# Kernel tuning notes

Measured on AMD Instinct MI355X. Metric: run time of the kernel, lower is better.

## Reference

```python
import jax, jax.numpy as jnp
import numpy as np

N = 50000   # nodes
E = 500000  # edges
F = 256     # node feature dim
ED = 64     # edge feature dim
H = 128     # hidden channels
O = 32      # out channels
NEG_SLOPE = 0.2
EPS = 1e-16


def setup_inputs() -> dict:
    key = jax.random.key(0)
    ks = jax.random.split(key, 16)
    s = 0.05
    return {
        "x": jax.random.normal(ks[0], (N, F), jnp.float32),
        "edge_index": jax.random.randint(ks[1], (2, E), 0, N, dtype=jnp.int32),
        "edge_attr": jax.random.normal(ks[2], (E, ED), jnp.float32),
        # layer 1 (embed): F -> H
        "W1": jax.random.normal(ks[3], (F, H), jnp.float32) * s,
        "att_src1": jax.random.normal(ks[4], (H,), jnp.float32) * s,
        "att_dst1": jax.random.normal(ks[5], (H,), jnp.float32) * s,
        "We1": jax.random.normal(ks[6], (ED, H), jnp.float32) * s,
        "att_edge1": jax.random.normal(ks[7], (H,), jnp.float32) * s,
        "b1": jnp.zeros((H,), jnp.float32),
        # layer 2 (classifier): H -> O
        "W2": jax.random.normal(ks[8], (H, O), jnp.float32) * s,
        "att_src2": jax.random.normal(ks[9], (O,), jnp.float32) * s,
        "att_dst2": jax.random.normal(ks[10], (O,), jnp.float32) * s,
        "We2": jax.random.normal(ks[11], (ED, O), jnp.float32) * s,
        "att_edge2": jax.random.normal(ks[12], (O,), jnp.float32) * s,
        "b2": jnp.zeros((O,), jnp.float32),
    }


def _add_self_loops_mean(src, dst, ea, n):
    # PyG add_self_loops(fill_value='mean'): self-loop edge_attr = mean of
    # incoming edge_attr per target node (0 for isolated nodes).
    ones = jnp.ones((ea.shape[0],), ea.dtype)
    cnt = jax.ops.segment_sum(ones, dst, num_segments=n)
    summ = jax.ops.segment_sum(ea, dst, num_segments=n)  # [n, ED]
    mean = summ / jnp.maximum(cnt, 1.0)[:, None]
    loop = jnp.arange(n, dtype=src.dtype)
    return (jnp.concatenate([src, loop]),
            jnp.concatenate([dst, loop]),
            jnp.concatenate([ea, mean], axis=0))


def _gat_conv(x, src, dst, ea, W, a_src, a_dst, We, a_edge, b):
    n = x.shape[0]
    src, dst, ea = _add_self_loops_mean(src, dst, ea, n)
    h = x @ W                       # [n, C]
    he = ea @ We                    # [E', C]
    a_s = h @ a_src                 # [n]
    a_d = h @ a_dst                 # [n]
    a_e = he @ a_edge               # [E']
    alpha = a_s[src] + a_d[dst] + a_e
    alpha = jax.nn.leaky_relu(alpha, NEG_SLOPE)
    # segment softmax over incoming edges of each target node
    m = jax.ops.segment_max(alpha, dst, num_segments=n)
    ex = jnp.exp(alpha - m[dst])
    denom = jax.ops.segment_sum(ex, dst, num_segments=n)
    coef = ex / (denom[dst] + EPS)
    out = jax.ops.segment_sum(coef[:, None] * h[src], dst, num_segments=n)
    return out + b


def reference(x, edge_index, edge_attr,
              W1, att_src1, att_dst1, We1, att_edge1, b1,
              W2, att_src2, att_dst2, We2, att_edge2, b2):
    src, dst = edge_index[0], edge_index[1]
    x1 = _gat_conv(x, src, dst, edge_attr, W1, att_src1, att_dst1, We1, att_edge1, b1)
    h = jax.nn.relu(x1)  # Dropout(0.5) is identity in eval mode
    out = _gat_conv(h, src, dst, edge_attr, W2, att_src2, att_dst2, We2, att_edge2, b2)
    return (out, h)
```

## Files before the change

### kernel.cpp

```cpp
#include <hip/hip_runtime.h>

#define N_NODES 50000
#define N_EDGES 500000
#define F_DIM 256
#define ED_DIM 64
#define H_DIM 128
#define O_DIM 32
#define NEG_SLOPE 0.2f
#define EPS_F 1e-16f

#define EB 2048

typedef __attribute__((ext_vector_type(8))) short short8;
typedef __attribute__((ext_vector_type(4))) float floatx4;

__device__ __forceinline__ unsigned short f2bf(float f) {
    union { float f; unsigned u; } c; c.f = f;
    unsigned u = c.u;
    return (unsigned short)((u + 0x7fffu + ((u >> 16) & 1u)) >> 16);
}
__device__ __forceinline__ float bf2f_lo(unsigned u) { return __uint_as_float(u << 16); }
__device__ __forceinline__ float bf2f_hi(unsigned u) { return __uint_as_float(u & 0xffff0000u); }
__device__ __forceinline__ float leaky(float a) { return a > 0.f ? a : a * NEG_SLOPE; }
__device__ __forceinline__ float dot4(float4 a, float4 b) {
    return a.x * b.x + a.y * b.y + a.z * b.z + a.w * b.w;
}

__global__ void k_prep(const float* __restrict__ We1, const float* __restrict__ aev1,
                       const float* __restrict__ We2, const float* __restrict__ aev2,
                       float* __restrict__ wv1, float* __restrict__ wv2,
                       const float* __restrict__ W1, const float* __restrict__ W2,
                       const float* __restrict__ as2v, const float* __restrict__ ad2v,
                       float* __restrict__ was2, float* __restrict__ wad2,
                       unsigned short* __restrict__ W1T, unsigned short* __restrict__ W2T,
                       int* __restrict__ cnt) {
    if (blockIdx.x == 32) {
        int t = threadIdx.x;
        if (t < 64) {
            float s = 0.f;
            for (int c = 0; c < H_DIM; c++) s += We1[t * H_DIM + c] * aev1[c];
            wv1[t] = s;
        } else if (t < 128) {
            int k = t - 64;
            float s = 0.f;
            for (int c = 0; c < O_DIM; c++) s += We2[k * O_DIM + c] * aev2[c];
            wv2[k] = s;
        } else {
            int c = t - 128;
            float s = 0.f, d = 0.f;
            for (int o = 0; o < O_DIM; o++) {
                float w = W2[c * O_DIM + o];
                s += w * as2v[o];
                d += w * ad2v[o];
            }
            was2[c] = s; wad2[c] = d;
        }
        return;
    }
    int gid = blockIdx.x * 256 + threadIdx.x;
    const int stride = 32 * 256;
    for (int i = gid; i < N_NODES; i += stride) cnt[i] = 0;
    for (int i = gid; i < H_DIM * F_DIM; i += stride) {
        int n = i >> 8, k = i & 255;
        W1T[i] = f2bf(W1[k * H_DIM + n]);
    }
    for (int i = gid; i < O_DIM * H_DIM; i += stride) {
        int n = i >> 7, k = i & 127;
        W2T[i] = f2bf(W2[k * O_DIM + n]);
    }
}

__global__ __launch_bounds__(256) void k_edge_ae(
        const float* __restrict__ ea, const int* __restrict__ dst,
        const float* __restrict__ wv1, const float* __restrict__ wv2,
        float2* __restrict__ ae12, int* __restrict__ cnt) {
    int tid = threadIdx.x;
    int wave = tid >> 6, lane = tid & 63;
    int sub = lane & 3, eg = lane >> 2;
    float4 w1[4], w2[4];
#pragma unroll
    for (int j = 0; j < 4; j++) {
        w1[j] = ((const float4*)wv1)[sub * 4 + j];
        w2[j] = ((const float4*)wv2)[sub * 4 + j];
    }
    int g0 = (blockIdx.x * 4 + wave) * 16 + eg;
    const int stride = EB * 64;
    for (int e = g0; e < N_EDGES; e += stride) {
        const float4* row = (const float4*)(ea + (size_t)e * ED_DIM + sub * 16);
        float4 q0 = row[0], q1 = row[1], q2 = row[2], q3 = row[3];
        float s1 = dot4(q0, w1[0]) + dot4(q1, w1[1]) + dot4(q2, w1[2]) + dot4(q3, w1[3]);
        float s2 = dot4(q0, w2[0]) + dot4(q1, w2[1]) + dot4(q2, w2[2]) + dot4(q3, w2[3]);
        s1 += __shfl_xor(s1, 1); s2 += __shfl_xor(s2, 1);
        s1 += __shfl_xor(s1, 2); s2 += __shfl_xor(s2, 2);
        if (sub == 0) {
            ae12[e] = make_float2(s1, s2);
            atomicAdd(&cnt[dst[e]], 1);
        }
    }
}

__global__ __launch_bounds__(256) void k_gemm1(const float* __restrict__ A,
        const unsigned short* __restrict__ BT,
        const float* __restrict__ asv, const float* __restrict__ adv,
        unsigned short* __restrict__ Hb, float* __restrict__ a_s, float* __restrict__ a_d, int M) {
    __shared__ unsigned short As[128 * 40];
    __shared__ unsigned short Bs[128 * 40];
    int tid = threadIdx.x;
    int wave = tid >> 6, lane = tid & 63;
    int q = lane >> 4, r = lane & 15;
    int bm0 = blockIdx.x * 128;
    floatx4 acc[2][8];
#pragma unroll
    for (int a = 0; a < 2; a++)
#pragma unroll
        for (int b = 0; b < 8; b++) acc[a][b] = (floatx4){0.f, 0.f, 0.f, 0.f};

    int rr = tid >> 3;
    int kc = tid & 7;
    for (int k0 = 0; k0 < 256; k0 += 32) {
#pragma unroll
        for (int i = 0; i < 4; i++) {
            int row = rr + 32 * i;
            int gr = bm0 + row;
            float4 v = make_float4(0.f, 0.f, 0.f, 0.f);
            if (gr < M) v = *(const float4*)(A + (size_t)gr * 256 + k0 + kc * 4);
            unsigned lo = (unsigned)f2bf(v.x) | ((unsigned)f2bf(v.y) << 16);
            unsigned hi = (unsigned)f2bf(v.z) | ((unsigned)f2bf(v.w) << 16);
            *(uint2*)&As[row * 40 + kc * 4] = make_uint2(lo, hi);
        }
#pragma unroll
        for (int i = 0; i < 2; i++) {
            int idx = tid + 256 * i;
            int n = idx >> 2, ck = idx & 3;
            *(uint4*)&Bs[n * 40 + ck * 8] = *(const uint4*)(BT + n * 256 + k0 + ck * 8);
        }
        __syncthreads();
        short8 af[2], bf[8];
#pragma unroll
        for (int rt = 0; rt < 2; rt++)
            af[rt] = *(const short8*)&As[(wave * 32 + rt * 16 + r) * 40 + q * 8];
#pragma unroll
        for (int nt = 0; nt < 8; nt++)
            bf[nt] = *(const short8*)&Bs[(nt * 16 + r) * 40 + q * 8];
#pragma unroll
        for (int rt = 0; rt < 2; rt++)
#pragma unroll
            for (int nt = 0; nt < 8; nt++)
                acc[rt][nt] = __builtin_amdgcn_mfma_f32_16x16x32_bf16(af[rt], bf[nt], acc[rt][nt], 0, 0, 0);
        __syncthreads();
    }
#pragma unroll
    for (int rt = 0; rt < 2; rt++) {
        int rowb = bm0 + wave * 32 + rt * 16 + q * 4;
        float ps[4] = {0.f, 0.f, 0.f, 0.f}, pd[4] = {0.f, 0.f, 0.f, 0.f};
#pragma unroll
        for (int nt = 0; nt < 8; nt++) {
            int col = nt * 16 + r;
            float av = asv[col], dv = adv[col];
#pragma unroll
            for (int reg = 0; reg < 4; reg++) {
                float v = acc[rt][nt][reg];
                if (rowb + reg < M) Hb[(size_t)(rowb + reg) * 128 + col] = f2bf(v);
                ps[reg] += v * av;
                pd[reg] += v * dv;
            }
        }
#pragma unroll
        for (int reg = 0; reg < 4; reg++) {
#pragma unroll
            for (int off = 1; off < 16; off <<= 1) {
                ps[reg] += __shfl_xor(ps[reg], off);
                pd[reg] += __shfl_xor(pd[reg], off);
            }
        }
        if (r == 0) {
#pragma unroll
            for (int reg = 0; reg < 4; reg++) {
                if (rowb + reg < M) { a_s[rowb + reg] = ps[reg]; a_d[rowb + reg] = pd[reg]; }
            }
        }
    }
}

__global__ void k_scan1(const int* __restrict__ cnt, int* __restrict__ bsum, int n) {
    __shared__ int sh[256];
    int b = blockIdx.x, t = threadIdx.x;
    int base = b * 1024;
    int s = 0;
    for (int j = 0; j < 4; j++) {
        int idx = base + t * 4 + j;
        if (idx < n) s += cnt[idx];
    }
    sh[t] = s; __syncthreads();
    for (int o = 128; o > 0; o >>= 1) {
        if (t < o) sh[t] += sh[t + o];
        __syncthreads();
    }
    if (t == 0) bsum[b] = sh[0];
}

__global__ void k_scan2(const int* __restrict__ bsum, int* __restrict__ bpre,
                        int* __restrict__ offs, int nb, int n) {
    if (threadIdx.x == 0) {
        int run = 0;
        for (int b = 0; b < nb; b++) { bpre[b] = run; run += bsum[b]; }
        offs[n] = run;
    }
}

__global__ void k_scan3(const int* __restrict__ cnt, const int* __restrict__ bpre,
                        int* __restrict__ offs, int* __restrict__ cursor, int n) {
    __shared__ int sh[256];
    int b = blockIdx.x, t = threadIdx.x;
    int base = b * 1024;
    int v[4]; int s = 0;
    for (int j = 0; j < 4; j++) {
        int idx = base + t * 4 + j;
        v[j] = (idx < n) ? cnt[idx] : 0;
        s += v[j];
    }
    sh[t] = s; __syncthreads();
    for (int o = 1; o < 256; o <<= 1) {
        int x = (t >= o) ? sh[t - o] : 0;
        __syncthreads();
        sh[t] += x;
        __syncthreads();
    }
    int texcl = sh[t] - s + bpre[b];
    int run = 0;
    for (int j = 0; j < 4; j++) {
        int idx = base + t * 4 + j;
        if (idx < n) { offs[idx] = texcl + run; cursor[idx] = texcl + run; }
        run += v[j];
    }
}

__global__ __launch_bounds__(256) void k_scatter(const int* __restrict__ src, const int* __restrict__ dst,
                          const float2* __restrict__ ae12, const float* __restrict__ a_s1,
                          int* __restrict__ cursor, float4* __restrict__ csr) {
    int e = blockIdx.x * blockDim.x + threadIdx.x;
    if (e >= N_EDGES) return;
    int s = src[e];
    int d = dst[e];
    float2 a = ae12[e];
    float as = a_s1[s];
    int p = atomicAdd(&cursor[d], 1);
    csr[p] = make_float4(__int_as_float(s), a.x, a.y, as);
}

template <bool RELU>
__global__ __launch_bounds__(256) void k_agg128(const unsigned short* __restrict__ h,
                         const float* __restrict__ a_s, const float* __restrict__ a_d,
                         const int* __restrict__ offs, const float4* __restrict__ csr,
                         const float* __restrict__ bias,
                         const float* __restrict__ was2, const float* __restrict__ wad2,
                         float* __restrict__ a_s2, float* __restrict__ a_d2,
                         float* __restrict__ out) {
    int wave = threadIdx.x >> 6, lane = threadIdx.x & 63;
    int i = blockIdx.x * 4 + wave;
    int r = lane & 15;
    int g = lane >> 4;
    int rs = offs[i], re = offs[i + 1];
    int deg = re - rs;
    float adl = a_d[i];
    float4 acc0 = {0.f, 0.f, 0.f, 0.f}, acc1 = {0.f, 0.f, 0.f, 0.f};
    float dsum = 0.f, sum_ae = 0.f;

#define P128(EL)                                                              \
    {                                                                         \
        float4 c = csr[EL];            \
        int s = __float_as_int(c.x);                                          \
        float aev = c.y;                                                      \
        float ex = __expf(leaky(c.w + adl + aev));                            \
        if (r == 0) { dsum += ex; sum_ae += aev; }                            \
        uint4 hv = *(const uint4*)(h + (size_t)s * 128 + r * 8);              \
        acc0.x += ex * bf2f_lo(hv.x); acc0.y += ex * bf2f_hi(hv.x);           \
        acc0.z += ex * bf2f_lo(hv.y); acc0.w += ex * bf2f_hi(hv.y);           \
        acc1.x += ex * bf2f_lo(hv.z); acc1.y += ex * bf2f_hi(hv.z);           \
        acc1.z += ex * bf2f_lo(hv.w); acc1.w += ex * bf2f_hi(hv.w);           \
    }

    int el = rs + g;
    for (; el + 4 < re; el += 8) { P128(el); P128(el + 4); }
    if (el < re) P128(el);
#undef P128

#pragma unroll
    for (int o = 1; o < 64; o <<= 1) {
        dsum += __shfl_xor(dsum, o);
        sum_ae += __shfl_xor(sum_ae, o);
    }

    float loop_ae = sum_ae / (float)(deg > 1 ? deg : 1);
    float al = leaky(a_s[i] + adl + loop_ae);
    float exs = __expf(al);
    float* a0 = (float*)&acc0; float* a1 = (float*)&acc1;
#pragma unroll
    for (int c = 0; c < 4; c++) {
        a0[c] += __shfl_xor(a0[c], 16); a0[c] += __shfl_xor(a0[c], 32);
        a1[c] += __shfl_xor(a1[c], 16); a1[c] += __shfl_xor(a1[c], 32);
    }
    if (g == 0) {
        float inv = 1.0f / (dsum + exs + EPS_F);
        uint4 hv = *(const uint4*)(h + (size_t)i * 128 + r * 8);
        const float4* bp = (const float4*)bias;
        float4 b0 = bp[r * 2], b1 = bp[r * 2 + 1];
        float4 o0, o1;
        o0.x = (a0[0] + exs * bf2f_lo(hv.x)) * inv + b0.x;
        o0.y = (a0[1] + exs * bf2f_hi(hv.x)) * inv + b0.y;
        o0.z = (a0[2] + exs * bf2f_lo(hv.y)) * inv + b0.z;
        o0.w = (a0[3] + exs * bf2f_hi(hv.y)) * inv + b0.w;
        o1.x = (a1[0] + exs * bf2f_lo(hv.z)) * inv + b1.x;
        o1.y = (a1[1] + exs * bf2f_hi(hv.z)) * inv + b1.y;
        o1.z = (a1[2] + exs * bf2f_lo(hv.w)) * inv + b1.z;
        o1.w = (a1[3] + exs * bf2f_hi(hv.w)) * inv + b1.w;
        if (RELU) {
            o0.x = fmaxf(o0.x, 0.f); o0.y = fmaxf(o0.y, 0.f); o0.z = fmaxf(o0.z, 0.f); o0.w = fmaxf(o0.w, 0.f);
            o1.x = fmaxf(o1.x, 0.f); o1.y = fmaxf(o1.y, 0.f); o1.z = fmaxf(o1.z, 0.f); o1.w = fmaxf(o1.w, 0.f);
        }
        float4* op = (float4*)(out + (size_t)i * 128);
        op[r * 2] = o0;
        op[r * 2 + 1] = o1;
        float4 wsa = ((const float4*)was2)[r * 2], wsb = ((const float4*)was2)[r * 2 + 1];
        float4 wda = ((const float4*)wad2)[r * 2], wdb = ((const float4*)wad2)[r * 2 + 1];
        float ps = dot4(o0, wsa) + dot4(o1, wsb);
        float pd = dot4(o0, wda) + dot4(o1, wdb);
#pragma unroll
        for (int o = 1; o < 16; o <<= 1) {
            ps += __shfl_xor(ps, o);
            pd += __shfl_xor(pd, o);
        }
        if (r == 0) { a_s2[i] = ps; a_d2[i] = pd; }
    }
}

__global__ __launch_bounds__(256) void k_gemm2(const float* __restrict__ A,
        const unsigned short* __restrict__ BT,
        unsigned short* __restrict__ Hb, int M) {
    __shared__ unsigned short As[128 * 40];
    __shared__ unsigned short Bs[32 * 40];
    int tid = threadIdx.x;
    int wave = tid >> 6, lane = tid & 63;
    int q = lane >> 4, r = lane & 15;
    int bm0 = blockIdx.x * 128;
    floatx4 acc[2][2];
#pragma unroll
    for (int a = 0; a < 2; a++)
#pragma unroll
        for (int b = 0; b < 2; b++) acc[a][b] = (floatx4){0.f, 0.f, 0.f, 0.f};

    int rr = tid >> 3;
    int kc = tid & 7;
    for (int k0 = 0; k0 < 128; k0 += 32) {
#pragma unroll
        for (int i = 0; i < 4; i++) {
            int row = rr + 32 * i;
            int gr = bm0 + row;
            float4 v = make_float4(0.f, 0.f, 0.f, 0.f);
            if (gr < M) v = *(const float4*)(A + (size_t)gr * 128 + k0 + kc * 4);
            unsigned lo = (unsigned)f2bf(v.x) | ((unsigned)f2bf(v.y) << 16);
            unsigned hi = (unsigned)f2bf(v.z) | ((unsigned)f2bf(v.w) << 16);
            *(uint2*)&As[row * 40 + kc * 4] = make_uint2(lo, hi);
        }
        if (tid < 128) {
            int n = tid >> 2, ck = tid & 3;
            *(uint4*)&Bs[n * 40 + ck * 8] = *(const uint4*)(BT + n * 128 + k0 + ck * 8);
        }
        __syncthreads();
        short8 af[2], bf[2];
#pragma unroll
        for (int rt = 0; rt < 2; rt++)
            af[rt] = *(const short8*)&As[(wave * 32 + rt * 16 + r) * 40 + q * 8];
#pragma unroll
        for (int nt = 0; nt < 2; nt++)
            bf[nt] = *(const short8*)&Bs[(nt * 16 + r) * 40 + q * 8];
#pragma unroll
        for (int rt = 0; rt < 2; rt++)
#pragma unroll
            for (int nt = 0; nt < 2; nt++)
                acc[rt][nt] = __builtin_amdgcn_mfma_f32_16x16x32_bf16(af[rt], bf[nt], acc[rt][nt], 0, 0, 0);
        __syncthreads();
    }
#pragma unroll
    for (int rt = 0; rt < 2; rt++) {
        int rowb = bm0 + wave * 32 + rt * 16 + q * 4;
#pragma unroll
        for (int nt = 0; nt < 2; nt++) {
            int col = nt * 16 + r;
#pragma unroll
            for (int reg = 0; reg < 4; reg++) {
                if (rowb + reg < M) Hb[(size_t)(rowb + reg) * 32 + col] = f2bf(acc[rt][nt][reg]);
            }
        }
    }
}

__global__ __launch_bounds__(256) void k_agg32(const unsigned short* __restrict__ h,
                        const float* __restrict__ a_s, const float* __restrict__ a_d,
                        const int* __restrict__ offs, const float4* __restrict__ csr,
                        const float* __restrict__ bias,
                        float* __restrict__ out) {
    int wave = threadIdx.x >> 6, lane = threadIdx.x & 63;
    int i = blockIdx.x * 4 + wave;
    int r = lane & 7;
    int g = lane >> 3;
    int rs = offs[i], re = offs[i + 1];
    int deg = re - rs;
    float adl = a_d[i];
    float4 acc = {0.f, 0.f, 0.f, 0.f};
    float dsum = 0.f, sum_ae = 0.f;

#define P32(EL)                                                               \
    {                                                                         \
        float4 c = csr[EL];                                                   \
        int s = __float_as_int(c.x);                                          \
        float aev = c.z;                                                      \
        float ex = __expf(leaky(a_s[s] + adl + aev));                         \
        if (r == 0) { dsum += ex; sum_ae += aev; }                            \
        uint2 hv = *(const uint2*)(h + (size_t)s * 32 + r * 4);               \
        acc.x += ex * bf2f_lo(hv.x); acc.y += ex * bf2f_hi(hv.x);             \
        acc.z += ex * bf2f_lo(hv.y); acc.w += ex * bf2f_hi(hv.y);             \
    }

    int el = rs + g;
    for (; el + 8 < re; el += 16) { P32(el); P32(el + 8); }
    if (el < re) P32(el);
#undef P32

#pragma unroll
    for (int o = 1; o < 64; o <<= 1) {
        dsum += __shfl_xor(dsum, o);
        sum_ae += __shfl_xor(sum_ae, o);
    }

    float loop_ae = sum_ae / (float)(deg > 1 ? deg : 1);
    float al = leaky(a_s[i] + adl + loop_ae);
    float exs = __expf(al);
#pragma unroll
    for (int o = 8; o < 64; o <<= 1) {
        acc.x += __shfl_xor(acc.x, o); acc.y += __shfl_xor(acc.y, o);
        acc.z += __shfl_xor(acc.z, o); acc.w += __shfl_xor(acc.w, o);
    }
    if (g == 0) {
        float inv = 1.0f / (dsum + exs + EPS_F);
        uint2 hv = *(const uint2*)(h + (size_t)i * 32 + r * 4);
        float4 bv = ((const float4*)bias)[r];
        float4 ov;
        ov.x = (acc.x + exs * bf2f_lo(hv.x)) * inv + bv.x;
        ov.y = (acc.y + exs * bf2f_hi(hv.x)) * inv + bv.y;
        ov.z = (acc.z + exs * bf2f_lo(hv.y)) * inv + bv.z;
        ov.w = (acc.w + exs * bf2f_hi(hv.y)) * inv + bv.w;
        ((float4*)(out + (size_t)i * 32))[r] = ov;
    }
}

extern "C" void kernel_launch(void* const* d_in, const int* in_sizes, int n_in,
                              void* d_out, int out_size, void* d_ws, size_t ws_size,
                              hipStream_t stream) {
    const float* x    = (const float*)d_in[0];
    const int* ei     = (const int*)d_in[1];
    const float* ea   = (const float*)d_in[2];
    const float* W1   = (const float*)d_in[3];
    const float* as1v = (const float*)d_in[4];
    const float* ad1v = (const float*)d_in[5];
    const float* We1  = (const float*)d_in[6];
    const float* aev1 = (const float*)d_in[7];
    const float* b1   = (const float*)d_in[8];
    const float* W2   = (const float*)d_in[9];
    const float* as2v = (const float*)d_in[10];
    const float* ad2v = (const float*)d_in[11];
    const float* We2  = (const float*)d_in[12];
    const float* aev2 = (const float*)d_in[13];
    const float* b2   = (const float*)d_in[14];

    const int* src = ei;
    const int* dst = ei + N_EDGES;

    char* w = (char*)d_ws;
    size_t off = 0;
    auto alloc = [&](size_t bytes) -> void* {
        void* p = w + off;
        off += bytes;
        off = (off + 255) & ~(size_t)255;
        return p;
    };
    unsigned short* h1b = (unsigned short*)alloc((size_t)N_NODES * H_DIM * 2);
    unsigned short* h2b = (unsigned short*)alloc((size_t)N_NODES * O_DIM * 2);
    float2* ae12   = (float2*)alloc((size_t)N_EDGES * 8);
    int* cnt       = (int*)alloc((size_t)N_NODES * 4);
    int* offs      = (int*)alloc((size_t)(N_NODES + 1) * 4);
    int* cursor    = (int*)alloc((size_t)N_NODES * 4);
    float4* csr    = (float4*)alloc((size_t)N_EDGES * 16);
    int* bsum      = (int*)alloc(64 * 4);
    int* bpre      = (int*)alloc(64 * 4);
    float* wv1     = (float*)alloc(64 * 4);
    float* wv2     = (float*)alloc(64 * 4);
    float* was2    = (float*)alloc(128 * 4);
    float* wad2    = (float*)alloc(128 * 4);
    float* a_s1    = (float*)alloc((size_t)N_NODES * 4);
    float* a_d1    = (float*)alloc((size_t)N_NODES * 4);
    float* a_s2    = (float*)alloc((size_t)N_NODES * 4);
    float* a_d2    = (float*)alloc((size_t)N_NODES * 4);
    unsigned short* W1T = (unsigned short*)alloc((size_t)H_DIM * F_DIM * 2);
    unsigned short* W2T = (unsigned short*)alloc((size_t)O_DIM * H_DIM * 2);

    k_prep<<<33, 256, 0, stream>>>(We1, aev1, We2, aev2, wv1, wv2, W1, W2,
                                   as2v, ad2v, was2, wad2, W1T, W2T, cnt);

    k_edge_ae<<<EB, 256, 0, stream>>>(ea, dst, wv1, wv2, ae12, cnt);

    k_gemm1<<<(N_NODES + 127) / 128, 256, 0, stream>>>(x, W1T, as1v, ad1v,
                                                       h1b, a_s1, a_d1, N_NODES);

    int nb = (N_NODES + 1023) / 1024;
    k_scan1<<<nb, 256, 0, stream>>>(cnt, bsum, N_NODES);
    k_scan2<<<1, 64, 0, stream>>>(bsum, bpre, offs, nb, N_NODES);
    k_scan3<<<nb, 256, 0, stream>>>(cnt, bpre, offs, cursor, N_NODES);

    k_scatter<<<(N_EDGES + 255) / 256, 256, 0, stream>>>(src, dst, ae12, a_s1,
                                                         cursor, csr);

    float* out = (float*)d_out;
    float* h_out = out + (size_t)N_NODES * O_DIM;

    k_agg128<true><<<(N_NODES + 3) / 4, 256, 0, stream>>>(h1b, a_s1, a_d1, offs,
                                                          csr, b1, was2, wad2,
                                                          a_s2, a_d2, h_out);

    k_gemm2<<<(N_NODES + 127) / 128, 256, 0, stream>>>(h_out, W2T, h2b, N_NODES);

    k_agg32<<<(N_NODES + 3) / 4, 256, 0, stream>>>(h2b, a_s2, a_d2, offs,
                                                   csr, b2, out);
}
```

Measured before the change: 379.3 us.

## Fuse second-layer GEMM into aggregation kernel and merge scan passes

The layer-2 projection (h @ W2) now happens inside the first aggregation kernel. W2 is staged in shared memory, each node's ReLU output goes through a per-wave shared buffer, and a dot product produces the bf16 h2 row directly, so the separate MFMA GEMM kernel and its re-read of h_out are gone. The aggregation kernels become persistent grid-stride loops over a fixed grid of 2048 blocks. The single-thread scan2 kernel is folded into scan3, with each block summing the earlier block totals through a wave shuffle. The fused GEMM runs as scalar FP32 FMAs instead of matrix cores, and it adds a block-wide barrier per node iteration.

```diff
diff --git a/kernel.cpp b/kernel.cpp
--- a/kernel.cpp
+++ b/kernel.cpp
@@ -10,6 +10,7 @@
 #define EPS_F 1e-16f
 
 #define EB 2048
+#define AB 2048
 
 typedef __attribute__((ext_vector_type(8))) short short8;
 typedef __attribute__((ext_vector_type(4))) float floatx4;
@@ -32,7 +33,7 @@
                        const float* __restrict__ W1, const float* __restrict__ W2,
                        const float* __restrict__ as2v, const float* __restrict__ ad2v,
                        float* __restrict__ was2, float* __restrict__ wad2,
-                       unsigned short* __restrict__ W1T, unsigned short* __restrict__ W2T,
+                       unsigned short* __restrict__ W1T,
                        int* __restrict__ cnt) {
     if (blockIdx.x == 32) {
         int t = threadIdx.x;
@@ -64,10 +65,6 @@
         int n = i >> 8, k = i & 255;
         W1T[i] = f2bf(W1[k * H_DIM + n]);
     }
-    for (int i = gid; i < O_DIM * H_DIM; i += stride) {
-        int n = i >> 7, k = i & 127;
-        W2T[i] = f2bf(W2[k * O_DIM + n]);
-    }
 }
 
 __global__ __launch_bounds__(256) void k_edge_ae(
@@ -199,25 +196,23 @@
     if (t == 0) bsum[b] = sh[0];
 }
 
-__global__ void k_scan2(const int* __restrict__ bsum, int* __restrict__ bpre,
-                        int* __restrict__ offs, int nb, int n) {
-    if (threadIdx.x == 0) {
-        int run = 0;
-        for (int b = 0; b < nb; b++) { bpre[b] = run; run += bsum[b]; }
-        offs[n] = run;
-    }
-}
-
-__global__ void k_scan3(const int* __restrict__ cnt, const int* __restrict__ bpre,
-                        int* __restrict__ offs, int* __restrict__ cursor, int n) {
+__global__ void k_scan3(const int* __restrict__ cnt, const int* __restrict__ bsum,
+                        int* __restrict__ offs, int* __restrict__ cursor, int n, int nb) {
     __shared__ int sh[256];
+    __shared__ int bpre_sh;
     int b = blockIdx.x, t = threadIdx.x;
+    if (t < 64) {
+        int v = (t < b) ? bsum[t] : 0;
+#pragma unroll
+        for (int o = 1; o < 64; o <<= 1) v += __shfl_xor(v, o);
+        if (t == 0) bpre_sh = v;
+    }
     int base = b * 1024;
-    int v[4]; int s = 0;
+    int v4[4]; int s = 0;
     for (int j = 0; j < 4; j++) {
         int idx = base + t * 4 + j;
-        v[j] = (idx < n) ? cnt[idx] : 0;
-        s += v[j];
+        v4[j] = (idx < n) ? cnt[idx] : 0;
+        s += v4[j];
     }
     sh[t] = s; __syncthreads();
     for (int o = 1; o < 256; o <<= 1) {
@@ -226,13 +221,14 @@
         sh[t] += x;
         __syncthreads();
     }
-    int texcl = sh[t] - s + bpre[b];
+    int texcl = sh[t] - s + bpre_sh;
     int run = 0;
     for (int j = 0; j < 4; j++) {
         int idx = base + t * 4 + j;
         if (idx < n) { offs[idx] = texcl + run; cursor[idx] = texcl + run; }
-        run += v[j];
-    }
+        run += v4[j];
+    }
+    if (b == nb - 1 && t == 255) offs[n] = bpre_sh + sh[255];
 }
 
 __global__ __launch_bounds__(256) void k_scatter(const int* __restrict__ src, const int* __restrict__ dst,
@@ -248,23 +244,32 @@
     csr[p] = make_float4(__int_as_float(s), a.x, a.y, as);
 }
 
-template <bool RELU>
 __global__ __launch_bounds__(256) void k_agg128(const unsigned short* __restrict__ h,
                          const float* __restrict__ a_s, const float* __restrict__ a_d,
                          const int* __restrict__ offs, const float4* __restrict__ csr,
                          const float* __restrict__ bias,
                          const float* __restrict__ was2, const float* __restrict__ wad2,
+                         const float* __restrict__ W2,
                          float* __restrict__ a_s2, float* __restrict__ a_d2,
+                         unsigned short* __restrict__ h2b,
                          float* __restrict__ out) {
-    int wave = threadIdx.x >> 6, lane = threadIdx.x & 63;
-    int i = blockIdx.x * 4 + wave;
+    __shared__ float W2s[128 * 32];
+    __shared__ float xsh[4][128];
+    int tid = threadIdx.x;
+    for (int idx = tid; idx < 128 * 32; idx += 256) W2s[idx] = W2[idx];
+    __syncthreads();
+    int wave = tid >> 6, lane = tid & 63;
     int r = lane & 15;
     int g = lane >> 4;
-    int rs = offs[i], re = offs[i + 1];
-    int deg = re - rs;
-    float adl = a_d[i];
-    float4 acc0 = {0.f, 0.f, 0.f, 0.f}, acc1 = {0.f, 0.f, 0.f, 0.f};
-    float dsum = 0.f, sum_ae = 0.f;
+    int ch = lane & 31, half = lane >> 5;
+
+    for (int i0 = blockIdx.x * 4; i0 < N_NODES; i0 += gridDim.x * 4) {
+        int i = i0 + wave;
+        int rs = offs[i], re = offs[i + 1];
+        int deg = re - rs;
+        float adl = a_d[i];
+        float4 acc0 = {0.f, 0.f, 0.f, 0.f}, acc1 = {0.f, 0.f, 0.f, 0.f};
+        float dsum = 0.f, sum_ae = 0.f;
 
 #define P128(EL)                                                              \
     {                                                                         \
@@ -280,117 +285,68 @@
         acc1.z += ex * bf2f_lo(hv.w); acc1.w += ex * bf2f_hi(hv.w);           \
     }
 
-    int el = rs + g;
-    for (; el + 4 < re; el += 8) { P128(el); P128(el + 4); }
-    if (el < re) P128(el);
+        int el = rs + g;
+        for (; el + 4 < re; el += 8) { P128(el); P128(el + 4); }
+        if (el < re) P128(el);
 #undef P128
 
 #pragma unroll
-    for (int o = 1; o < 64; o <<= 1) {
-        dsum += __shfl_xor(dsum, o);
-        sum_ae += __shfl_xor(sum_ae, o);
-    }
-
-    float loop_ae = sum_ae / (float)(deg > 1 ? deg : 1);
-    float al = leaky(a_s[i] + adl + loop_ae);
-    float exs = __expf(al);
-    float* a0 = (float*)&acc0; float* a1 = (float*)&acc1;
-#pragma unroll
-    for (int c = 0; c < 4; c++) {
-        a0[c] += __shfl_xor(a0[c], 16); a0[c] += __shfl_xor(a0[c], 32);
-        a1[c] += __shfl_xor(a1[c], 16); a1[c] += __shfl_xor(a1[c], 32);
-    }
-    if (g == 0) {
-        float inv = 1.0f / (dsum + exs + EPS_F);
-        uint4 hv = *(const uint4*)(h + (size_t)i * 128 + r * 8);
-        const float4* bp = (const float4*)bias;
-        float4 b0 = bp[r * 2], b1 = bp[r * 2 + 1];
-        float4 o0, o1;
-        o0.x = (a0[0] + exs * bf2f_lo(hv.x)) * inv + b0.x;
-        o0.y = (a0[1] + exs * bf2f_hi(hv.x)) * inv + b0.y;
-        o0.z = (a0[2] + exs * bf2f_lo(hv.y)) * inv + b0.z;
-        o0.w = (a0[3] + exs * bf2f_hi(hv.y)) * inv + b0.w;
-        o1.x = (a1[0] + exs * bf2f_lo(hv.z)) * inv + b1.x;
-        o1.y = (a1[1] + exs * bf2f_hi(hv.z)) * inv + b1.y;
-        o1.z = (a1[2] + exs * bf2f_lo(hv.w)) * inv + b1.z;
-        o1.w = (a1[3] + exs * bf2f_hi(hv.w)) * inv + b1.w;
-        if (RELU) {
+        for (int o = 1; o < 64; o <<= 1) {
+            dsum += __shfl_xor(dsum, o);
+            sum_ae += __shfl_xor(sum_ae, o);
+        }
+
+        float loop_ae = sum_ae / (float)(deg > 1 ? deg : 1);
+        float al = leaky(a_s[i] + adl + loop_ae);
+        float exs = __expf(al);
+        float* a0 = (float*)&acc0; float* a1 = (float*)&acc1;
+#pragma unroll
+        for (int c = 0; c < 4; c++) {
+            a0[c] += __shfl_xor(a0[c], 16); a0[c] += __shfl_xor(a0[c], 32);
+            a1[c] += __shfl_xor(a1[c], 16); a1[c] += __shfl_xor(a1[c], 32);
+        }
+        if (g == 0) {
+            float inv = 1.0f / (dsum + exs + EPS_F);
+            uint4 hv = *(const uint4*)(h + (size_t)i * 128 + r * 8);
+            const float4* bp = (const float4*)bias;
+            float4 b0 = bp[r * 2], b1 = bp[r * 2 + 1];
+            float4 o0, o1;
+            o0.x = (a0[0] + exs * bf2f_lo(hv.x)) * inv + b0.x;
+            o0.y = (a0[1] + exs * bf2f_hi(hv.x)) * inv + b0.y;
+            o0.z = (a0[2] + exs * bf2f_lo(hv.y)) * inv + b0.z;
+            o0.w = (a0[3] + exs * bf2f_hi(hv.y)) * inv + b0.w;
+            o1.x = (a1[0] + exs * bf2f_lo(hv.z)) * inv + b1.x;
+            o1.y = (a1[1] + exs * bf2f_hi(hv.z)) * inv + b1.y;
+            o1.z = (a1[2] + exs * bf2f_lo(hv.w)) * inv + b1.z;
+            o1.w = (a1[3] + exs * bf2f_hi(hv.w)) * inv + b1.w;
             o0.x = fmaxf(o0.x, 0.f); o0.y = fmaxf(o0.y, 0.f); o0.z = fmaxf(o0.z, 0.f); o0.w = fmaxf(o0.w, 0.f);
             o1.x = fmaxf(o1.x, 0.f); o1.y = fmaxf(o1.y, 0.f); o1.z = fmaxf(o1.z, 0.f); o1.w = fmaxf(o1.w, 0.f);
-        }
-        float4* op = (float4*)(out + (size_t)i * 128);
-        op[r * 2] = o0;
-        op[r * 2 + 1] = o1;
-        float4 wsa = ((const float4*)was2)[r * 2], wsb = ((const float4*)was2)[r * 2 + 1];
-        float4 wda = ((const float4*)wad2)[r * 2], wdb = ((const float4*)wad2)[r * 2 + 1];
-        float ps = dot4(o0, wsa) + dot4(o1, wsb);
-        float pd = dot4(o0, wda) + dot4(o1, wdb);
-#pragma unroll
-        for (int o = 1; o < 16; o <<= 1) {
-            ps += __shfl_xor(ps, o);
-            pd += __shfl_xor(pd, o);
-        }
-        if (r == 0) { a_s2[i] = ps; a_d2[i] = pd; }
-    }
-}
-
-__global__ __launch_bounds__(256) void k_gemm2(const float* __restrict__ A,
-        const unsigned short* __restrict__ BT,
-        unsigned short* __restrict__ Hb, int M) {
-    __shared__ unsigned short As[128 * 40];
-    __shared__ unsigned short Bs[32 * 40];
-    int tid = threadIdx.x;
-    int wave = tid >> 6, lane = tid & 63;
-    int q = lane >> 4, r = lane & 15;
-    int bm0 = blockIdx.x * 128;
-    floatx4 acc[2][2];
-#pragma unroll
-    for (int a = 0; a < 2; a++)
-#pragma unroll
-        for (int b = 0; b < 2; b++) acc[a][b] = (floatx4){0.f, 0.f, 0.f, 0.f};
-
-    int rr = tid >> 3;
-    int kc = tid & 7;
-    for (int k0 = 0; k0 < 128; k0 += 32) {
-#pragma unroll
-        for (int i = 0; i < 4; i++) {
-            int row = rr + 32 * i;
-            int gr = bm0 + row;
-            float4 v = make_float4(0.f, 0.f, 0.f, 0.f);
-            if (gr < M) v = *(const float4*)(A + (size_t)gr * 128 + k0 + kc * 4);
-            unsigned lo = (unsigned)f2bf(v.x) | ((unsigned)f2bf(v.y) << 16);
-            unsigned hi = (unsigned)f2bf(v.z) | ((unsigned)f2bf(v.w) << 16);
-            *(uint2*)&As[row * 40 + kc * 4] = make_uint2(lo, hi);
-        }
-        if (tid < 128) {
-            int n = tid >> 2, ck = tid & 3;
-            *(uint4*)&Bs[n * 40 + ck * 8] = *(const uint4*)(BT + n * 128 + k0 + ck * 8);
-        }
-        __syncthreads();
-        short8 af[2], bf[2];
-#pragma unroll
-        for (int rt = 0; rt < 2; rt++)
-            af[rt] = *(const short8*)&As[(wave * 32 + rt * 16 + r) * 40 + q * 8];
-#pragma unroll
-        for (int nt = 0; nt < 2; nt++)
-            bf[nt] = *(const short8*)&Bs[(nt * 16 + r) * 40 + q * 8];
-#pragma unroll
-        for (int rt = 0; rt < 2; rt++)
-#pragma unroll
-            for (int nt = 0; nt < 2; nt++)
-                acc[rt][nt] = __builtin_amdgcn_mfma_f32_16x16x32_bf16(af[rt], bf[nt], acc[rt][nt], 0, 0, 0);
-        __syncthreads();
-    }
-#pragma unroll
-    for (int rt = 0; rt < 2; rt++) {
-        int rowb = bm0 + wave * 32 + rt * 16 + q * 4;
-#pragma unroll
-        for (int nt = 0; nt < 2; nt++) {
-            int col = nt * 16 + r;
-#pragma unroll
-            for (int reg = 0; reg < 4; reg++) {
-                if (rowb + reg < M) Hb[(size_t)(rowb + reg) * 32 + col] = f2bf(acc[rt][nt][reg]);
+            float4* op = (float4*)(out + (size_t)i * 128);
+            op[r * 2] = o0;
+            op[r * 2 + 1] = o1;
+            float* xr = xsh[wave];
+            xr[r * 8 + 0] = o0.x; xr[r * 8 + 1] = o0.y; xr[r * 8 + 2] = o0.z; xr[r * 8 + 3] = o0.w;
+            xr[r * 8 + 4] = o1.x; xr[r * 8 + 5] = o1.y; xr[r * 8 + 6] = o1.z; xr[r * 8 + 7] = o1.w;
+            float4 wsa = ((const float4*)was2)[r * 2], wsb = ((const float4*)was2)[r * 2 + 1];
+            float4 wda = ((const float4*)wad2)[r * 2], wdb = ((const float4*)wad2)[r * 2 + 1];
+            float ps = dot4(o0, wsa) + dot4(o1, wsb);
+            float pd = dot4(o0, wda) + dot4(o1, wdb);
+#pragma unroll
+            for (int o = 1; o < 16; o <<= 1) {
+                ps += __shfl_xor(ps, o);
+                pd += __shfl_xor(pd, o);
             }
+            if (r == 0) { a_s2[i] = ps; a_d2[i] = pd; }
+        }
+        __syncthreads();
+        {
+            const float* xr = xsh[wave];
+            float p = 0.f;
+            const float* wp = W2s + (half * 64) * 32 + ch;
+#pragma unroll 8
+            for (int c = 0; c < 64; c++) p += xr[half * 64 + c] * wp[c * 32];
+            p += __shfl_xor(p, 32);
+            if (lane < 32) h2b[(size_t)i * 32 + ch] = f2bf(p);
         }
     }
 }
@@ -401,14 +357,15 @@
                         const float* __restrict__ bias,
                         float* __restrict__ out) {
     int wave = threadIdx.x >> 6, lane = threadIdx.x & 63;
-    int i = blockIdx.x * 4 + wave;
     int r = lane & 7;
     int g = lane >> 3;
-    int rs = offs[i], re = offs[i + 1];
-    int deg = re - rs;
-    float adl = a_d[i];
-    float4 acc = {0.f, 0.f, 0.f, 0.f};
-    float dsum = 0.f, sum_ae = 0.f;
+    for (int i0 = blockIdx.x * 4; i0 < N_NODES; i0 += gridDim.x * 4) {
+        int i = i0 + wave;
+        int rs = offs[i], re = offs[i + 1];
+        int deg = re - rs;
+        float adl = a_d[i];
+        float4 acc = {0.f, 0.f, 0.f, 0.f};
+        float dsum = 0.f, sum_ae = 0.f;
 
 #define P32(EL)                                                               \
     {                                                                         \
@@ -422,35 +379,36 @@
         acc.z += ex * bf2f_lo(hv.y); acc.w += ex * bf2f_hi(hv.y);             \
     }
 
-    int el = rs + g;
-    for (; el + 8 < re; el += 16) { P32(el); P32(el + 8); }
-    if (el < re) P32(el);
+        int el = rs + g;
+        for (; el + 8 < re; el += 16) { P32(el); P32(el + 8); }
+        if (el < re) P32(el);
 #undef P32
 
 #pragma unroll
-    for (int o = 1; o < 64; o <<= 1) {
-        dsum += __shfl_xor(dsum, o);
-        sum_ae += __shfl_xor(sum_ae, o);
-    }
-
-    float loop_ae = sum_ae / (float)(deg > 1 ? deg : 1);
-    float al = leaky(a_s[i] + adl + loop_ae);
-    float exs = __expf(al);
-#pragma unroll
-    for (int o = 8; o < 64; o <<= 1) {
-        acc.x += __shfl_xor(acc.x, o); acc.y += __shfl_xor(acc.y, o);
-        acc.z += __shfl_xor(acc.z, o); acc.w += __shfl_xor(acc.w, o);
-    }
-    if (g == 0) {
-        float inv = 1.0f / (dsum + exs + EPS_F);
-        uint2 hv = *(const uint2*)(h + (size_t)i * 32 + r * 4);
-        float4 bv = ((const float4*)bias)[r];
-        float4 ov;
-        ov.x = (acc.x + exs * bf2f_lo(hv.x)) * inv + bv.x;
-        ov.y = (acc.y + exs * bf2f_hi(hv.x)) * inv + bv.y;
-        ov.z = (acc.z + exs * bf2f_lo(hv.y)) * inv + bv.z;
-        ov.w = (acc.w + exs * bf2f_hi(hv.y)) * inv + bv.w;
-        ((float4*)(out + (size_t)i * 32))[r] = ov;
+        for (int o = 1; o < 64; o <<= 1) {
+            dsum += __shfl_xor(dsum, o);
+            sum_ae += __shfl_xor(sum_ae, o);
+        }
+
+        float loop_ae = sum_ae / (float)(deg > 1 ? deg : 1);
+        float al = leaky(a_s[i] + adl + loop_ae);
+        float exs = __expf(al);
+#pragma unroll
+        for (int o = 8; o < 64; o <<= 1) {
+            acc.x += __shfl_xor(acc.x, o); acc.y += __shfl_xor(acc.y, o);
+            acc.z += __shfl_xor(acc.z, o); acc.w += __shfl_xor(acc.w, o);
+        }
+        if (g == 0) {
+            float inv = 1.0f / (dsum + exs + EPS_F);
+            uint2 hv = *(const uint2*)(h + (size_t)i * 32 + r * 4);
+            float4 bv = ((const float4*)bias)[r];
+            float4 ov;
+            ov.x = (acc.x + exs * bf2f_lo(hv.x)) * inv + bv.x;
+            ov.y = (acc.y + exs * bf2f_hi(hv.x)) * inv + bv.y;
+            ov.z = (acc.z + exs * bf2f_lo(hv.y)) * inv + bv.z;
+            ov.w = (acc.w + exs * bf2f_hi(hv.y)) * inv + bv.w;
+            ((float4*)(out + (size_t)i * 32))[r] = ov;
+        }
     }
 }
 
@@ -492,7 +450,6 @@
     int* cursor    = (int*)alloc((size_t)N_NODES * 4);
     float4* csr    = (float4*)alloc((size_t)N_EDGES * 16);
     int* bsum      = (int*)alloc(64 * 4);
-    int* bpre      = (int*)alloc(64 * 4);
     float* wv1     = (float*)alloc(64 * 4);
     float* wv2     = (float*)alloc(64 * 4);
     float* was2    = (float*)alloc(128 * 4);
@@ -502,10 +459,9 @@
     float* a_s2    = (float*)alloc((size_t)N_NODES * 4);
     float* a_d2    = (float*)alloc((size_t)N_NODES * 4);
     unsigned short* W1T = (unsigned short*)alloc((size_t)H_DIM * F_DIM * 2);
-    unsigned short* W2T = (unsigned short*)alloc((size_t)O_DIM * H_DIM * 2);
 
     k_prep<<<33, 256, 0, stream>>>(We1, aev1, We2, aev2, wv1, wv2, W1, W2,
-                                   as2v, ad2v, was2, wad2, W1T, W2T, cnt);
+                                   as2v, ad2v, was2, wad2, W1T, cnt);
 
     k_edge_ae<<<EB, 256, 0, stream>>>(ea, dst, wv1, wv2, ae12, cnt);
 
@@ -514,8 +470,7 @@
 
     int nb = (N_NODES + 1023) / 1024;
     k_scan1<<<nb, 256, 0, stream>>>(cnt, bsum, N_NODES);
-    k_scan2<<<1, 64, 0, stream>>>(bsum, bpre, offs, nb, N_NODES);
-    k_scan3<<<nb, 256, 0, stream>>>(cnt, bpre, offs, cursor, N_NODES);
+    k_scan3<<<nb, 256, 0, stream>>>(cnt, bsum, offs, cursor, N_NODES, nb);
 
     k_scatter<<<(N_EDGES + 255) / 256, 256, 0, stream>>>(src, dst, ae12, a_s1,
                                                          cursor, csr);
@@ -523,12 +478,8 @@
     float* out = (float*)d_out;
     float* h_out = out + (size_t)N_NODES * O_DIM;
 
-    k_agg128<true><<<(N_NODES + 3) / 4, 256, 0, stream>>>(h1b, a_s1, a_d1, offs,
-                                                          csr, b1, was2, wad2,
-                                                          a_s2, a_d2, h_out);
-
-    k_gemm2<<<(N_NODES + 127) / 128, 256, 0, stream>>>(h_out, W2T, h2b, N_NODES);
-
-    k_agg32<<<(N_NODES + 3) / 4, 256, 0, stream>>>(h2b, a_s2, a_d2, offs,
-                                                   csr, b2, out);
-}
+    k_agg128<<<AB, 256, 0, stream>>>(h1b, a_s1, a_d1, offs, csr, b1,
+                                     was2, wad2, W2, a_s2, a_d2, h2b, h_out);
+
+    k_agg32<<<AB, 256, 0, stream>>>(h2b, a_s2, a_d2, offs, csr, b2, out);
+}
```

Result: slower. 396.2 us (+4.4%).
